# Performance work log

Hardware: AMD Instinct MI355X
Metric: run time of the kernel (lower is better)

The kernel has to match this reference:

```python
import jax, jax.numpy as jnp
import numpy as np

NB, DIM, DSTATE, DCONV, EXPAND = 4, 256, 16, 4, 2
DIN = EXPAND * DIM                 # 512
DTRANK = (DIM + 15) // 16          # 16, mamba-ssm default dt_rank = ceil(d_model/16)
B, L = 16, 512


def layer_norm(x, w, b, eps=1e-5):
    mu = x.mean(-1, keepdims=True)
    var = x.var(-1, keepdims=True)
    return (x - mu) * jax.lax.rsqrt(var + eps) * w + b


def selective_scan(u, delta, A, Bm, Cm, D):
    # u, delta: (B,L,DIN); Bm,Cm: (B,L,N); A: (DIN,N); D: (DIN,)
    def step(h, xs):
        d_t, B_t, C_t, u_t = xs          # (B,DIN), (B,N), (B,N), (B,DIN)
        dA = jnp.exp(d_t[..., None] * A)                                  # (B,DIN,N)
        h = dA * h + d_t[..., None] * B_t[:, None, :] * u_t[..., None]   # (B,DIN,N)
        y = jnp.einsum('bdn,bn->bd', h, C_t)
        return h, y

    h0 = jnp.zeros((u.shape[0], u.shape[2], A.shape[1]), u.dtype)
    xs = (delta.transpose(1, 0, 2), Bm.transpose(1, 0, 2),
          Cm.transpose(1, 0, 2), u.transpose(1, 0, 2))
    _, ys = jax.lax.scan(step, h0, xs)
    return ys.transpose(1, 0, 2) + u * D


def mamba_block(x, ln_w, ln_b, in_w, in_b, cw, cb, xp_w, dtw, dtb, A_log, D, ow):
    h = layer_norm(x, ln_w, ln_b)
    xz = h @ in_w.T + in_b                       # (B,L,2*DIN)
    xin, z = xz[..., :DIN], xz[..., DIN:]
    # causal depthwise conv over the sequence dim
    xc = jax.lax.conv_general_dilated(
        xin.transpose(0, 2, 1), cw[:, None, :], (1,), [(DCONV - 1, 0)],
        dimension_numbers=('NCH', 'OIH', 'NCH'), feature_group_count=DIN)
    xc = jax.nn.silu(xc + cb[None, :, None]).transpose(0, 2, 1)   # (B,L,DIN)
    dbc = xc @ xp_w.T                                             # (B,L,DTRANK+2*N)
    dt = jax.nn.softplus(dbc[..., :DTRANK] @ dtw.T + dtb)         # (B,L,DIN)
    Bm = dbc[..., DTRANK:DTRANK + DSTATE]
    Cm = dbc[..., DTRANK + DSTATE:]
    y = selective_scan(xc, dt, -jnp.exp(A_log), Bm, Cm, D)
    return x + (y * jax.nn.silu(z)) @ ow.T       # dropout = identity at eval


def setup_inputs() -> dict:
    key = jax.random.key(0)
    ks = jax.random.split(key, 8)
    s = 0.02
    A_log = jnp.tile(jnp.log(jnp.arange(1, DSTATE + 1, dtype=jnp.float32))[None, None, :],
                     (NB, DIN, 1))
    return {
        'x': jax.random.normal(ks[0], (B, L, DIM), jnp.float32),
        'ln_w': jnp.ones((NB, DIM), jnp.float32),
        'ln_b': jnp.zeros((NB, DIM), jnp.float32),
        'in_proj_w': jax.random.normal(ks[1], (NB, 2 * DIN, DIM), jnp.float32) * s,
        'in_proj_b': jnp.zeros((NB, 2 * DIN), jnp.float32),
        'conv_w': jax.random.normal(ks[2], (NB, DIN, DCONV), jnp.float32) * s,
        'conv_b': jnp.zeros((NB, DIN), jnp.float32),
        'x_proj_w': jax.random.normal(ks[3], (NB, DTRANK + 2 * DSTATE, DIN), jnp.float32) * s,
        'dt_proj_w': jax.random.normal(ks[4], (NB, DIN, DTRANK), jnp.float32) * s,
        'dt_proj_b': jax.random.uniform(ks[5], (NB, DIN), jnp.float32, -4.0, -3.0),
        'A_log': A_log,
        'D': jnp.ones((NB, DIN), jnp.float32),
        'out_proj_w': jax.random.normal(ks[6], (NB, DIM, DIN), jnp.float32) * s,
    }


def reference(x, ln_w, ln_b, in_proj_w, in_proj_b, conv_w, conv_b, x_proj_w,
              dt_proj_w, dt_proj_b, A_log, D, out_proj_w):
    for i in range(NB):
        x = mamba_block(x, ln_w[i], ln_b[i], in_proj_w[i], in_proj_b[i],
                        conv_w[i], conv_b[i], x_proj_w[i], dt_proj_w[i],
                        dt_proj_b[i], A_log[i], D[i], out_proj_w[i])
    return x
```

## Files before the change

### kernel.cpp

```cpp
#include <hip/hip_runtime.h>
#include <math.h>

#define NB 4
#define DIMM 256
#define DSTATE 16
#define DCONV 4
#define DIN 512
#define DTRANK 16
#define BB 16
#define LL 512
#define TT (BB * LL)
#define XZ_DIM (2 * DIN)
#define DBC_DIM (DTRANK + 2 * DSTATE)
#define NC 32
#define CHUNK (LL / NC)

__device__ __forceinline__ unsigned short f2bf(float f) {
    union { float f; unsigned int u; } v; v.f = f;
    unsigned int r = v.u + 0x7fff + ((v.u >> 16) & 1);
    return (unsigned short)(r >> 16);
}
__device__ __forceinline__ float bf2f(unsigned short u) {
    union { unsigned int i; float f; } v; v.i = ((unsigned int)u) << 16;
    return v.f;
}

__global__ __launch_bounds__(256) void cvt3_kernel(const float* __restrict__ s1,
                                                   unsigned short* __restrict__ d1, int n1,
                                                   const float* __restrict__ s2,
                                                   unsigned short* __restrict__ d2, int n2,
                                                   const float* __restrict__ s3,
                                                   unsigned short* __restrict__ d3, int n3) {
    int stride = gridDim.x * 256;
    for (int i = blockIdx.x * 256 + threadIdx.x; i < n1; i += stride) {
        float4 v = ((const float4*)s1)[i];
        ushort4 o; o.x = f2bf(v.x); o.y = f2bf(v.y); o.z = f2bf(v.z); o.w = f2bf(v.w);
        ((ushort4*)d1)[i] = o;
    }
    for (int i = blockIdx.x * 256 + threadIdx.x; i < n2; i += stride) {
        float4 v = ((const float4*)s2)[i];
        ushort4 o; o.x = f2bf(v.x); o.y = f2bf(v.y); o.z = f2bf(v.z); o.w = f2bf(v.w);
        ((ushort4*)d2)[i] = o;
    }
    for (int i = blockIdx.x * 256 + threadIdx.x; i < n3; i += stride) {
        float4 v = ((const float4*)s3)[i];
        ushort4 o; o.x = f2bf(v.x); o.y = f2bf(v.y); o.z = f2bf(v.z); o.w = f2bf(v.w);
        ((ushort4*)d3)[i] = o;
    }
}

__global__ __launch_bounds__(256) void ln_kernel(const float* __restrict__ x,
                                                 const float* __restrict__ w,
                                                 const float* __restrict__ bvec,
                                                 unsigned short* __restrict__ out) {
    int t = blockIdx.x;
    int i = threadIdx.x;
    float v = x[t * DIMM + i];
    float s = v, s2 = v * v;
#pragma unroll
    for (int off = 1; off < 64; off <<= 1) {
        s  += __shfl_xor(s, off);
        s2 += __shfl_xor(s2, off);
    }
    __shared__ float ss[4], ss2[4];
    int wid = i >> 6;
    if ((i & 63) == 0) { ss[wid] = s; ss2[wid] = s2; }
    __syncthreads();
    s  = ss[0] + ss[1] + ss[2] + ss[3];
    s2 = ss2[0] + ss2[1] + ss2[2] + ss2[3];
    float mu  = s * (1.0f / DIMM);
    float var = s2 * (1.0f / DIMM) - mu * mu;
    float r   = rsqrtf(var + 1e-5f);
    out[t * DIMM + i] = f2bf((v - mu) * r * w[i] + bvec[i]);
}

#define GBM2 128
#define GBN2 128
#define GBK2 32
#define LDW2 (GBK2 + 8)
__global__ __launch_bounds__(256) void gemm128(const unsigned short* __restrict__ A, int lda,
                                               const unsigned short* __restrict__ Bw, int ldb,
                                               const float* __restrict__ bias,
                                               unsigned short* __restrict__ C1b,
                                               unsigned short* __restrict__ C2b, int nsplit,
                                               int ldc, int K) {
    using short8  = __attribute__((ext_vector_type(8))) short;
    using floatx4 = __attribute__((ext_vector_type(4))) float;
    __shared__ __align__(16) unsigned short As[GBM2 * LDW2];
    __shared__ __align__(16) unsigned short Bs[GBN2 * LDW2];

    int tid  = threadIdx.x;
    int m0   = blockIdx.y * GBM2;
    int n0   = blockIdx.x * GBN2;
    int w    = tid >> 6;
    int lane = tid & 63;
    int wm   = (w & 1) * 64;
    int wn   = (w >> 1) * 64;
    int lr   = lane & 15;
    int quad = lane >> 4;

    floatx4 acc[4][4] = {};

    int ar = tid >> 1;
    int ak = (tid & 1) * 16;

    for (int k0 = 0; k0 < K; k0 += GBK2) {
        {
            const unsigned short* src = &A[(size_t)(m0 + ar) * lda + k0 + ak];
            int4 a0 = *(const int4*)(src);
            int4 a1 = *(const int4*)(src + 8);
            *(int4*)&As[ar * LDW2 + ak]     = a0;
            *(int4*)&As[ar * LDW2 + ak + 8] = a1;
        }
        {
            const unsigned short* src = &Bw[(size_t)(n0 + ar) * ldb + k0 + ak];
            int4 b0 = *(const int4*)(src);
            int4 b1 = *(const int4*)(src + 8);
            *(int4*)&Bs[ar * LDW2 + ak]     = b0;
            *(int4*)&Bs[ar * LDW2 + ak + 8] = b1;
        }
        __syncthreads();
        short8 af[4], bf[4];
#pragma unroll
        for (int i = 0; i < 4; ++i)
            af[i] = *(const short8*)&As[(wm + i * 16 + lr) * LDW2 + quad * 8];
#pragma unroll
        for (int j = 0; j < 4; ++j)
            bf[j] = *(const short8*)&Bs[(wn + j * 16 + lr) * LDW2 + quad * 8];
#pragma unroll
        for (int i = 0; i < 4; ++i)
#pragma unroll
            for (int j = 0; j < 4; ++j)
                acc[i][j] = __builtin_amdgcn_mfma_f32_16x16x32_bf16(af[i], bf[j], acc[i][j], 0, 0, 0);
        __syncthreads();
    }

#pragma unroll
    for (int j = 0; j < 4; ++j) {
        int cn = n0 + wn + j * 16 + lr;
        float bb = bias ? bias[cn] : 0.0f;
        unsigned short* dst = (cn < nsplit) ? C1b : C2b;
        int col = (cn < nsplit) ? cn : cn - nsplit;
#pragma unroll
        for (int i = 0; i < 4; ++i)
#pragma unroll
            for (int r = 0; r < 4; ++r) {
                int cm = m0 + wm + i * 16 + quad * 4 + r;
                dst[(size_t)cm * ldc + col] = f2bf(acc[i][j][r] + bb);
            }
    }
}

#define TBM 128
#define TBN 64
#define TBK 32
#define LDKW (TBK + 8)
__global__ __launch_bounds__(256) void gemm_bf16(const unsigned short* __restrict__ A, int lda,
                                                 const unsigned short* __restrict__ Bw, int ldb,
                                                 const float* __restrict__ bias,
                                                 const float* __restrict__ resid,
                                                 float* __restrict__ C,
                                                 unsigned short* __restrict__ C1b,
                                                 unsigned short* __restrict__ C2b, int nsplit,
                                                 int ldc, int N, int K) {
    using short8  = __attribute__((ext_vector_type(8))) short;
    using floatx4 = __attribute__((ext_vector_type(4))) float;
    __shared__ __align__(16) unsigned short As[TBM * LDKW];
    __shared__ __align__(16) unsigned short Bs[TBN * LDKW];

    int tid  = threadIdx.x;
    int m0   = blockIdx.y * TBM;
    int n0   = blockIdx.x * TBN;
    int w    = tid >> 6;
    int lane = tid & 63;
    int wm   = (w & 1) * 64;
    int wn   = (w >> 1) * 32;
    int lr   = lane & 15;
    int quad = lane >> 4;

    floatx4 acc[4][2] = {};

    int ar = tid >> 1;
    int ak = (tid & 1) * 16;
    int br = tid >> 2;
    int bk = (tid & 3) * 8;

    for (int k0 = 0; k0 < K; k0 += TBK) {
        {
            const unsigned short* src = &A[(size_t)(m0 + ar) * lda + k0 + ak];
            int4 a0 = *(const int4*)(src);
            int4 a1 = *(const int4*)(src + 8);
            *(int4*)&As[ar * LDKW + ak]     = a0;
            *(int4*)&As[ar * LDKW + ak + 8] = a1;
        }
        {
            int gn = n0 + br;
            int4 b0 = make_int4(0, 0, 0, 0);
            if (gn < N) b0 = *(const int4*)&Bw[(size_t)gn * ldb + k0 + bk];
            *(int4*)&Bs[br * LDKW + bk] = b0;
        }
        __syncthreads();
        short8 af[4], bf[2];
#pragma unroll
        for (int i = 0; i < 4; ++i)
            af[i] = *(const short8*)&As[(wm + i * 16 + lr) * LDKW + quad * 8];
#pragma unroll
        for (int j = 0; j < 2; ++j)
            bf[j] = *(const short8*)&Bs[(wn + j * 16 + lr) * LDKW + quad * 8];
#pragma unroll
        for (int i = 0; i < 4; ++i)
#pragma unroll
            for (int j = 0; j < 2; ++j)
                acc[i][j] = __builtin_amdgcn_mfma_f32_16x16x32_bf16(af[i], bf[j], acc[i][j], 0, 0, 0);
        __syncthreads();
    }

#pragma unroll
    for (int j = 0; j < 2; ++j) {
        int cn = n0 + wn + j * 16 + lr;
        if (cn < N) {
            float bb = bias ? bias[cn] : 0.0f;
            if (C1b) {
                unsigned short* dst = (cn < nsplit) ? C1b : C2b;
                int col = (cn < nsplit) ? cn : cn - nsplit;
#pragma unroll
                for (int i = 0; i < 4; ++i)
#pragma unroll
                    for (int r = 0; r < 4; ++r) {
                        int cm = m0 + wm + i * 16 + quad * 4 + r;
                        dst[(size_t)cm * ldc + col] = f2bf(acc[i][j][r] + bb);
                    }
            } else {
#pragma unroll
                for (int i = 0; i < 4; ++i)
#pragma unroll
                    for (int r = 0; r < 4; ++r) {
                        int cm = m0 + wm + i * 16 + quad * 4 + r;
                        float v = acc[i][j][r] + bb;
                        if (resid) v += resid[(size_t)cm * ldc + cn];
                        C[(size_t)cm * ldc + cn] = v;
                    }
            }
        }
    }
}

__global__ __launch_bounds__(256) void conv_silu(const unsigned short* __restrict__ Xb,
                                                 const float* __restrict__ cw,
                                                 const float* __restrict__ cb,
                                                 unsigned short* __restrict__ xcb) {
    int idx = blockIdx.x * blockDim.x + threadIdx.x;
    int d = idx & (DIN - 1);
    int t = idx >> 9;
    int l = t & (LL - 1);
    int bq = t >> 9;
    float acc = cb[d];
#pragma unroll
    for (int k = 0; k < DCONV; ++k) {
        int ls = l - (DCONV - 1) + k;
        if (ls >= 0) acc += cw[d * DCONV + k] * bf2f(Xb[(size_t)(bq * LL + ls) * DIN + d]);
    }
    float v = acc / (1.0f + __expf(-acc));
    xcb[(size_t)t * DIN + d] = f2bf(v);
}

__global__ __launch_bounds__(256) void dt_kernel(const float* __restrict__ dbc,
                                                 const float* __restrict__ dtw,
                                                 const float* __restrict__ dtbias,
                                                 unsigned short* __restrict__ dtout) {
    int idx = blockIdx.x * blockDim.x + threadIdx.x;
    int d = idx & (DIN - 1);
    int t = idx >> 9;
    float a = dtbias[d];
    const float4* wv = (const float4*)(dtw + d * DTRANK);
    const float* dr = dbc + (size_t)t * DBC_DIM;
#pragma unroll
    for (int q = 0; q < 4; ++q) {
        float4 w4 = wv[q];
        a += w4.x * dr[q * 4 + 0] + w4.y * dr[q * 4 + 1] +
             w4.z * dr[q * 4 + 2] + w4.w * dr[q * 4 + 3];
    }
    float sp = (a > 20.0f) ? a : log1pf(__expf(a));
    dtout[(size_t)t * DIN + d] = f2bf(sp);
}

__global__ __launch_bounds__(256) void scan_p1(const unsigned short* __restrict__ xcb,
                                               const unsigned short* __restrict__ dtb,
                                               const float* __restrict__ dbc,
                                               const float* __restrict__ A_log,
                                               float* __restrict__ S,
                                               float* __restrict__ H) {
    int bid = blockIdx.x;
    int dq = bid & 3;
    int c  = (bid >> 2) & (NC - 1);
    int b  = bid >> 7;
    int dloc = threadIdx.x >> 1;
    int sh   = threadIdx.x & 1;
    int d  = dq * 128 + dloc;
    int n0 = sh * 8;
    int base = b * LL + c * CHUNK;

    __shared__ float LB[CHUNK * DBC_DIM];
    for (int i = threadIdx.x; i < CHUNK * DBC_DIM / 4; i += 256)
        ((float4*)LB)[i] = ((const float4*)(dbc + (size_t)base * DBC_DIM))[i];

    float a[8];
    {
        const float4* ar = (const float4*)(A_log + d * DSTATE + n0);
        float4 v0 = ar[0], v1 = ar[1];
        a[0] = -__expf(v0.x); a[1] = -__expf(v0.y); a[2] = -__expf(v0.z); a[3] = -__expf(v0.w);
        a[4] = -__expf(v1.x); a[5] = -__expf(v1.y); a[6] = -__expf(v1.z); a[7] = -__expf(v1.w);
    }
    __syncthreads();

    float h[8];
#pragma unroll
    for (int j = 0; j < 8; ++j) h[j] = 0.0f;
    float Ssum = 0.0f;
    float u   = bf2f(xcb[(size_t)base * DIN + d]);
    float dtv = bf2f(dtb[(size_t)base * DIN + d]);
#pragma unroll 4
    for (int s = 0; s < CHUNK; ++s) {
        float nu  = bf2f(xcb[(size_t)(base + s + 1) * DIN + d]);
        float ndt = bf2f(dtb[(size_t)(base + s + 1) * DIN + d]);
        const float* row = &LB[s * DBC_DIM];
        float4 b0 = *(const float4*)&row[DTRANK + n0];
        float4 b1 = *(const float4*)&row[DTRANK + n0 + 4];
        const float btv[8] = {b0.x, b0.y, b0.z, b0.w, b1.x, b1.y, b1.z, b1.w};
        Ssum += dtv;
        float wv = dtv * u;
#pragma unroll
        for (int j = 0; j < 8; ++j) {
            float dA = __expf(dtv * a[j]);
            h[j] = dA * h[j] + wv * btv[j];
        }
        u = nu; dtv = ndt;
    }
    size_t sc = (size_t)b * NC + c;
    if (sh == 0) S[sc * DIN + d] = Ssum;
#pragma unroll
    for (int j = 0; j < 8; ++j) H[(sc * DIN + d) * 16 + n0 + j] = h[j];
}

__global__ __launch_bounds__(256) void scan_p2(const float* __restrict__ A_log,
                                               const float* __restrict__ S,
                                               float* __restrict__ H) {
    int idx = blockIdx.x * 256 + threadIdx.x;
    int n = idx & 15;
    int d = (idx >> 4) & (DIN - 1);
    int b = idx >> 13;
    float a = -__expf(A_log[d * DSTATE + n]);
    float h = 0.0f;
#pragma unroll
    for (int c = 0; c < NC; ++c) {
        size_t sc = (size_t)b * NC + c;
        float Sv = S[sc * DIN + d];
        size_t q = (sc * DIN + d) * 16 + n;
        float Hc = H[q];
        H[q] = h;
        h = __expf(a * Sv) * h + Hc;
    }
}

__global__ __launch_bounds__(256) void scan_p3(const unsigned short* __restrict__ xcb,
                                               const unsigned short* __restrict__ dtb,
                                               const unsigned short* __restrict__ Zb,
                                               const float* __restrict__ dbc,
                                               const float* __restrict__ A_log,
                                               const float* __restrict__ Dp,
                                               const float* __restrict__ Hin,
                                               unsigned short* __restrict__ gb) {
    int bid = blockIdx.x;
    int dq = bid & 3;
    int c  = (bid >> 2) & (NC - 1);
    int b  = bid >> 7;
    int dloc = threadIdx.x >> 1;
    int sh   = threadIdx.x & 1;
    int d  = dq * 128 + dloc;
    int n0 = sh * 8;
    int base = b * LL + c * CHUNK;

    __shared__ float LB[CHUNK * DBC_DIM];
    for (int i = threadIdx.x; i < CHUNK * DBC_DIM / 4; i += 256)
        ((float4*)LB)[i] = ((const float4*)(dbc + (size_t)base * DBC_DIM))[i];

    float a[8];
    {
        const float4* ar = (const float4*)(A_log + d * DSTATE + n0);
        float4 v0 = ar[0], v1 = ar[1];
        a[0] = -__expf(v0.x); a[1] = -__expf(v0.y); a[2] = -__expf(v0.z); a[3] = -__expf(v0.w);
        a[4] = -__expf(v1.x); a[5] = -__expf(v1.y); a[6] = -__expf(v1.z); a[7] = -__expf(v1.w);
    }
    float Dd = Dp[d];
    size_t sc = (size_t)b * NC + c;
    float h[8];
#pragma unroll
    for (int j = 0; j < 8; ++j) h[j] = Hin[(sc * DIN + d) * 16 + n0 + j];
    __syncthreads();

    float u   = bf2f(xcb[(size_t)base * DIN + d]);
    float dtv = bf2f(dtb[(size_t)base * DIN + d]);
#pragma unroll 4
    for (int s = 0; s < CHUNK; ++s) {
        float nu  = bf2f(xcb[(size_t)(base + s + 1) * DIN + d]);
        float ndt = bf2f(dtb[(size_t)(base + s + 1) * DIN + d]);
        const float* row = &LB[s * DBC_DIM];
        float4 b0 = *(const float4*)&row[DTRANK + n0];
        float4 b1 = *(const float4*)&row[DTRANK + n0 + 4];
        float4 c0 = *(const float4*)&row[DTRANK + DSTATE + n0];
        float4 c1 = *(const float4*)&row[DTRANK + DSTATE + n0 + 4];
        const float btv[8] = {b0.x, b0.y, b0.z, b0.w, b1.x, b1.y, b1.z, b1.w};
        const float ctv[8] = {c0.x, c0.y, c0.z, c0.w, c1.x, c1.y, c1.z, c1.w};
        float wv = dtv * u;
        float y  = (sh == 0) ? u * Dd : 0.0f;
#pragma unroll
        for (int j = 0; j < 8; ++j) {
            float dA = __expf(dtv * a[j]);
            h[j] = dA * h[j] + wv * btv[j];
            y += h[j] * ctv[j];
        }
        y += __shfl_xor(y, 1);
        if (sh == 0) {
            float zf = bf2f(Zb[(size_t)(base + s) * DIN + d]);
            float g = y * (zf / (1.0f + __expf(-zf)));
            gb[(size_t)(base + s) * DIN + d] = f2bf(g);
        }
        u = nu; dtv = ndt;
    }
}

extern "C" void kernel_launch(void* const* d_in, const int* in_sizes, int n_in,
                              void* d_out, int out_size, void* d_ws, size_t ws_size,
                              hipStream_t stream) {
    const float* x_in   = (const float*)d_in[0];
    const float* ln_w   = (const float*)d_in[1];
    const float* ln_b   = (const float*)d_in[2];
    const float* in_w   = (const float*)d_in[3];
    const float* in_b   = (const float*)d_in[4];
    const float* conv_w = (const float*)d_in[5];
    const float* conv_b = (const float*)d_in[6];
    const float* xp_w   = (const float*)d_in[7];
    const float* dt_w   = (const float*)d_in[8];
    const float* dt_b   = (const float*)d_in[9];
    const float* A_log  = (const float*)d_in[10];
    const float* Dp     = (const float*)d_in[11];
    const float* ow     = (const float*)d_in[12];
    float* out = (float*)d_out;

    const size_t M = 1048576;
    float* ws = (float*)d_ws;
    float* xbuf = ws;
    unsigned short* hb  = (unsigned short*)(ws + 2 * M);
    float* dbc = ws + 3 * M;
    unsigned short* Xb  = (unsigned short*)(ws + 4 * M);
    unsigned short* Zb  = (unsigned short*)(ws + 6 * M);
    unsigned short* xcb = (unsigned short*)(ws + 8 * M);
    unsigned short* dtb = (unsigned short*)(ws + 10 * M);
    unsigned short* gb  = (unsigned short*)(ws + 12 * M);
    float* Hbuf = ws + 14 * M;
    float* Sbuf = ws + 18 * M;
    unsigned short* inwb = (unsigned short*)(ws + 18 * M + 262144);
    unsigned short* owb  = inwb + (size_t)NB * XZ_DIM * DIMM;
    unsigned short* xpwb = owb + (size_t)NB * DIMM * DIN;

    cvt3_kernel<<<256, 256, 0, stream>>>(
        in_w, inwb, NB * XZ_DIM * DIMM / 4,
        ow,   owb,  NB * DIMM * DIN / 4,
        xp_w, xpwb, NB * DBC_DIM * DIN / 4);

    for (int layer = 0; layer < NB; ++layer) {
        const float* xi = (layer == 0) ? x_in : xbuf;
        float* xo = (layer == NB - 1) ? out : xbuf;

        ln_kernel<<<TT, 256, 0, stream>>>(xi, ln_w + layer * DIMM, ln_b + layer * DIMM, hb);

        gemm128<<<dim3(XZ_DIM / GBN2, TT / GBM2), 256, 0, stream>>>(
            hb, DIMM, inwb + (size_t)layer * XZ_DIM * DIMM, DIMM,
            in_b + layer * XZ_DIM, Xb, Zb, DIN, DIN, DIMM);

        conv_silu<<<(TT * DIN) / 256, 256, 0, stream>>>(
            Xb, conv_w + layer * DIN * DCONV, conv_b + layer * DIN, xcb);

        gemm_bf16<<<dim3(1, TT / TBM), 256, 0, stream>>>(
            xcb, DIN, xpwb + (size_t)layer * DBC_DIM * DIN, DIN,
            nullptr, nullptr, dbc, nullptr, nullptr, 0, DBC_DIM, DBC_DIM, DIN);

        dt_kernel<<<(TT * DIN) / 256, 256, 0, stream>>>(
            dbc, dt_w + (size_t)layer * DIN * DTRANK, dt_b + layer * DIN, dtb);

        const float* Al = A_log + (size_t)layer * DIN * DSTATE;
        scan_p1<<<BB * NC * 4, 256, 0, stream>>>(xcb, dtb, dbc, Al, Sbuf, Hbuf);
        scan_p2<<<(BB * DIN * 16) / 256, 256, 0, stream>>>(Al, Sbuf, Hbuf);
        scan_p3<<<BB * NC * 4, 256, 0, stream>>>(xcb, dtb, Zb, dbc, Al,
                                                 Dp + layer * DIN, Hbuf, gb);

        gemm_bf16<<<dim3(DIMM / TBN, TT / TBM), 256, 0, stream>>>(
            gb, DIN, owb + (size_t)layer * DIMM * DIN, DIN,
            nullptr, xi, xo, nullptr, nullptr, 0, DIMM, DIMM, DIN);
    }
}
```

Measured before the change: 679.3 us.

## Fuse conv+SiLU, x_proj GEMM and dt projection into one kernel; vectorize layernorm

Replaces the separate conv_silu, x_proj gemm_bf16 and dt_kernel launches with a single kernel. Each block handles 64 tokens: it computes the causal conv plus SiLU into shared memory, feeds those rows to MFMA for the 48-column x_proj, then computes dt with softplus from the shared dt-rank slice. This removes two launches and the global round trip of xcb into the GEMM and dbc into the dt step. Layernorm now handles one token per wavefront with float4 loads and no shared-memory reduction. The cost is a fused kernel with only 128 blocks and a serial dt loop over 64 tokens per thread, so parallelism is reduced.

```diff
diff --git a/kernel.cpp b/kernel.cpp
--- a/kernel.cpp
+++ b/kernel.cpp
@@ -49,29 +49,32 @@
     }
 }
 
-__global__ __launch_bounds__(256) void ln_kernel(const float* __restrict__ x,
-                                                 const float* __restrict__ w,
-                                                 const float* __restrict__ bvec,
-                                                 unsigned short* __restrict__ out) {
-    int t = blockIdx.x;
-    int i = threadIdx.x;
-    float v = x[t * DIMM + i];
-    float s = v, s2 = v * v;
+__global__ __launch_bounds__(256) void ln_kernel2(const float* __restrict__ x,
+                                                  const float* __restrict__ w,
+                                                  const float* __restrict__ bvec,
+                                                  unsigned short* __restrict__ out) {
+    int wid  = threadIdx.x >> 6;
+    int lane = threadIdx.x & 63;
+    int t = blockIdx.x * 4 + wid;
+    float4 v = *(const float4*)&x[(size_t)t * DIMM + lane * 4];
+    float s  = v.x + v.y + v.z + v.w;
+    float s2 = v.x * v.x + v.y * v.y + v.z * v.z + v.w * v.w;
 #pragma unroll
     for (int off = 1; off < 64; off <<= 1) {
         s  += __shfl_xor(s, off);
         s2 += __shfl_xor(s2, off);
     }
-    __shared__ float ss[4], ss2[4];
-    int wid = i >> 6;
-    if ((i & 63) == 0) { ss[wid] = s; ss2[wid] = s2; }
-    __syncthreads();
-    s  = ss[0] + ss[1] + ss[2] + ss[3];
-    s2 = ss2[0] + ss2[1] + ss2[2] + ss2[3];
     float mu  = s * (1.0f / DIMM);
     float var = s2 * (1.0f / DIMM) - mu * mu;
     float r   = rsqrtf(var + 1e-5f);
-    out[t * DIMM + i] = f2bf((v - mu) * r * w[i] + bvec[i]);
+    float4 w4 = *(const float4*)&w[lane * 4];
+    float4 b4 = *(const float4*)&bvec[lane * 4];
+    ushort4 o;
+    o.x = f2bf((v.x - mu) * r * w4.x + b4.x);
+    o.y = f2bf((v.y - mu) * r * w4.y + b4.y);
+    o.z = f2bf((v.z - mu) * r * w4.z + b4.z);
+    o.w = f2bf((v.w - mu) * r * w4.w + b4.w);
+    *(ushort4*)&out[(size_t)t * DIMM + lane * 4] = o;
 }
 
 #define GBM2 128
@@ -245,43 +248,122 @@
     }
 }
 
-__global__ __launch_bounds__(256) void conv_silu(const unsigned short* __restrict__ Xb,
+#define FBM 64
+#define FLDW 40
+__global__ __launch_bounds__(256) void fused_cxd(const unsigned short* __restrict__ Xb,
                                                  const float* __restrict__ cw,
                                                  const float* __restrict__ cb,
-                                                 unsigned short* __restrict__ xcb) {
-    int idx = blockIdx.x * blockDim.x + threadIdx.x;
-    int d = idx & (DIN - 1);
-    int t = idx >> 9;
-    int l = t & (LL - 1);
-    int bq = t >> 9;
-    float acc = cb[d];
-#pragma unroll
-    for (int k = 0; k < DCONV; ++k) {
-        int ls = l - (DCONV - 1) + k;
-        if (ls >= 0) acc += cw[d * DCONV + k] * bf2f(Xb[(size_t)(bq * LL + ls) * DIN + d]);
-    }
-    float v = acc / (1.0f + __expf(-acc));
-    xcb[(size_t)t * DIN + d] = f2bf(v);
-}
-
-__global__ __launch_bounds__(256) void dt_kernel(const float* __restrict__ dbc,
+                                                 const unsigned short* __restrict__ Bw,
                                                  const float* __restrict__ dtw,
                                                  const float* __restrict__ dtbias,
-                                                 unsigned short* __restrict__ dtout) {
-    int idx = blockIdx.x * blockDim.x + threadIdx.x;
-    int d = idx & (DIN - 1);
-    int t = idx >> 9;
-    float a = dtbias[d];
-    const float4* wv = (const float4*)(dtw + d * DTRANK);
-    const float* dr = dbc + (size_t)t * DBC_DIM;
-#pragma unroll
-    for (int q = 0; q < 4; ++q) {
-        float4 w4 = wv[q];
-        a += w4.x * dr[q * 4 + 0] + w4.y * dr[q * 4 + 1] +
-             w4.z * dr[q * 4 + 2] + w4.w * dr[q * 4 + 3];
-    }
-    float sp = (a > 20.0f) ? a : log1pf(__expf(a));
-    dtout[(size_t)t * DIN + d] = f2bf(sp);
+                                                 unsigned short* __restrict__ xcb,
+                                                 float* __restrict__ dbc,
+                                                 unsigned short* __restrict__ dtb) {
+    using short8  = __attribute__((ext_vector_type(8))) short;
+    using floatx4 = __attribute__((ext_vector_type(4))) float;
+    __shared__ __align__(16) unsigned short Xs[(FBM + 3) * 32];
+    __shared__ __align__(16) unsigned short As[FBM * FLDW];
+    __shared__ __align__(16) unsigned short Bs[48 * FLDW];
+    __shared__ float LBD[FBM * DTRANK];
+
+    int tid  = threadIdx.x;
+    int m0   = blockIdx.x * FBM;
+    int seq0 = m0 & ~(LL - 1);
+    int w    = tid >> 6;
+    int lane = tid & 63;
+    int lr   = lane & 15;
+    int quad = lane >> 4;
+    int wm   = w * 16;
+
+    int dl = tid & 31;
+    int tb = tid >> 5;
+
+    floatx4 acc[3] = {};
+
+    for (int it = 0; it < 16; ++it) {
+        int dc = it * 32;
+        __syncthreads();
+        for (int i = tid; i < (FBM + 3) * 4; i += 256) {
+            int row = i >> 2, off = (i & 3) * 8;
+            int gr = m0 - 3 + row;
+            int4 vv = make_int4(0, 0, 0, 0);
+            if (gr >= seq0) vv = *(const int4*)&Xb[(size_t)gr * DIN + dc + off];
+            *(int4*)&Xs[row * 32 + off] = vv;
+        }
+        for (int i = tid; i < 48 * 4; i += 256) {
+            int row = i >> 2, off = (i & 3) * 8;
+            *(int4*)&Bs[row * FLDW + off] = *(const int4*)&Bw[(size_t)row * DIN + dc + off];
+        }
+        __syncthreads();
+        {
+            int d = dc + dl;
+            float4 c4 = *(const float4*)&cw[d * 4];
+            float cbv = cb[d];
+#pragma unroll
+            for (int p = 0; p < 8; ++p) {
+                int t = tb + p * 8;
+                float a = cbv
+                    + c4.x * bf2f(Xs[(t + 0) * 32 + dl])
+                    + c4.y * bf2f(Xs[(t + 1) * 32 + dl])
+                    + c4.z * bf2f(Xs[(t + 2) * 32 + dl])
+                    + c4.w * bf2f(Xs[(t + 3) * 32 + dl]);
+                float v = a / (1.0f + __expf(-a));
+                unsigned short h = f2bf(v);
+                As[t * FLDW + dl] = h;
+                xcb[(size_t)(m0 + t) * DIN + d] = h;
+            }
+        }
+        __syncthreads();
+        short8 af  = *(const short8*)&As[(wm + lr) * FLDW + quad * 8];
+        short8 bf0 = *(const short8*)&Bs[(0 * 16 + lr) * FLDW + quad * 8];
+        short8 bf1 = *(const short8*)&Bs[(1 * 16 + lr) * FLDW + quad * 8];
+        short8 bf2v = *(const short8*)&Bs[(2 * 16 + lr) * FLDW + quad * 8];
+        acc[0] = __builtin_amdgcn_mfma_f32_16x16x32_bf16(af, bf0,  acc[0], 0, 0, 0);
+        acc[1] = __builtin_amdgcn_mfma_f32_16x16x32_bf16(af, bf1,  acc[1], 0, 0, 0);
+        acc[2] = __builtin_amdgcn_mfma_f32_16x16x32_bf16(af, bf2v, acc[2], 0, 0, 0);
+    }
+    __syncthreads();
+#pragma unroll
+    for (int j = 0; j < 3; ++j) {
+        int cn = j * 16 + lr;
+#pragma unroll
+        for (int r = 0; r < 4; ++r) {
+            int row = wm + quad * 4 + r;
+            float v = acc[j][r];
+            dbc[(size_t)(m0 + row) * DBC_DIM + cn] = v;
+            if (j == 0) LBD[row * DTRANK + cn] = v;
+        }
+    }
+    __syncthreads();
+    {
+        int d0 = tid * 2;
+        const float4* w0 = (const float4*)&dtw[(size_t)d0 * DTRANK];
+        const float4* w1 = (const float4*)&dtw[(size_t)(d0 + 1) * DTRANK];
+        float4 wa0 = w0[0], wa1 = w0[1], wa2 = w0[2], wa3 = w0[3];
+        float4 wb0 = w1[0], wb1 = w1[1], wb2 = w1[2], wb3 = w1[3];
+        float b0 = dtbias[d0], b1 = dtbias[d0 + 1];
+        for (int t = 0; t < FBM; ++t) {
+            const float* row = &LBD[t * DTRANK];
+            float4 r0 = *(const float4*)&row[0];
+            float4 r1 = *(const float4*)&row[4];
+            float4 r2 = *(const float4*)&row[8];
+            float4 r3 = *(const float4*)&row[12];
+            float a0 = b0;
+            a0 += wa0.x * r0.x + wa0.y * r0.y + wa0.z * r0.z + wa0.w * r0.w;
+            a0 += wa1.x * r1.x + wa1.y * r1.y + wa1.z * r1.z + wa1.w * r1.w;
+            a0 += wa2.x * r2.x + wa2.y * r2.y + wa2.z * r2.z + wa2.w * r2.w;
+            a0 += wa3.x * r3.x + wa3.y * r3.y + wa3.z * r3.z + wa3.w * r3.w;
+            float a1 = b1;
+            a1 += wb0.x * r0.x + wb0.y * r0.y + wb0.z * r0.z + wb0.w * r0.w;
+            a1 += wb1.x * r1.x + wb1.y * r1.y + wb1.z * r1.z + wb1.w * r1.w;
+            a1 += wb2.x * r2.x + wb2.y * r2.y + wb2.z * r2.z + wb2.w * r2.w;
+            a1 += wb3.x * r3.x + wb3.y * r3.y + wb3.z * r3.z + wb3.w * r3.w;
+            float sp0 = (a0 > 20.0f) ? a0 : log1pf(__expf(a0));
+            float sp1 = (a1 > 20.0f) ? a1 : log1pf(__expf(a1));
+            ushort2 o; o.x = f2bf(sp0); o.y = f2bf(sp1);
+            *(ushort2*)&dtb[(size_t)(m0 + t) * DIN + d0] = o;
+        }
+    }
 }
 
 __global__ __launch_bounds__(256) void scan_p1(const unsigned short* __restrict__ xcb,
@@ -472,21 +554,17 @@
         const float* xi = (layer == 0) ? x_in : xbuf;
         float* xo = (layer == NB - 1) ? out : xbuf;
 
-        ln_kernel<<<TT, 256, 0, stream>>>(xi, ln_w + layer * DIMM, ln_b + layer * DIMM, hb);
+        ln_kernel2<<<TT / 4, 256, 0, stream>>>(xi, ln_w + layer * DIMM, ln_b + layer * DIMM, hb);
 
         gemm128<<<dim3(XZ_DIM / GBN2, TT / GBM2), 256, 0, stream>>>(
             hb, DIMM, inwb + (size_t)layer * XZ_DIM * DIMM, DIMM,
             in_b + layer * XZ_DIM, Xb, Zb, DIN, DIN, DIMM);
 
-        conv_silu<<<(TT * DIN) / 256, 256, 0, stream>>>(
-            Xb, conv_w + layer * DIN * DCONV, conv_b + layer * DIN, xcb);
-
-        gemm_bf16<<<dim3(1, TT / TBM), 256, 0, stream>>>(
-            xcb, DIN, xpwb + (size_t)layer * DBC_DIM * DIN, DIN,
-            nullptr, nullptr, dbc, nullptr, nullptr, 0, DBC_DIM, DBC_DIM, DIN);
-
-        dt_kernel<<<(TT * DIN) / 256, 256, 0, stream>>>(
-            dbc, dt_w + (size_t)layer * DIN * DTRANK, dt_b + layer * DIN, dtb);
+        fused_cxd<<<TT / FBM, 256, 0, stream>>>(
+            Xb, conv_w + layer * DIN * DCONV, conv_b + layer * DIN,
+            xpwb + (size_t)layer * DBC_DIM * DIN,
+            dt_w + (size_t)layer * DIN * DTRANK, dt_b + layer * DIN,
+            xcb, dbc, dtb);
 
         const float* Al = A_log + (size_t)layer * DIN * DSTATE;
         scan_p1<<<BB * NC * 4, 256, 0, stream>>>(xcb, dtb, dbc, Al, Sbuf, Hbuf);
```

New measurement: 755.5 us. 1.11x slower.
